# Kernel optimization log

Measured on AMD Instinct MI355X. Metric: run time of the kernel, lower is better.

The kernel has to match this reference:

```python
import jax, jax.numpy as jnp
import numpy as np

QK_DIM = 1024
V_DIM = 1024
NUM_HEADS = 16
HEAD_DIM = 64
INNER = NUM_HEADS * HEAD_DIM  # 1024
SCALE = HEAD_DIM ** -0.5


def setup_inputs() -> dict:
    key = jax.random.key(0)
    ks = jax.random.split(key, 8)
    m, nq, nkv = 4, 2048, 2048
    xq = jax.random.normal(ks[0], (m, nq, QK_DIM), dtype=jnp.float32)
    xk = jax.random.normal(ks[1], (m, nkv, QK_DIM), dtype=jnp.float32)
    xv = jax.random.normal(ks[2], (m, nkv, V_DIM), dtype=jnp.float32)
    # torch nn.Linear weights are [out, in]; y = x @ W.T
    s_qk = (QK_DIM) ** -0.5
    s_in = (INNER) ** -0.5
    Wq = jax.random.uniform(ks[3], (INNER, QK_DIM), jnp.float32, -s_qk, s_qk)
    Wk = jax.random.uniform(ks[4], (INNER, QK_DIM), jnp.float32, -s_qk, s_qk)
    Wv = jax.random.uniform(ks[5], (INNER, V_DIM), jnp.float32, -s_qk, s_qk)
    Wo = jax.random.uniform(ks[6], (V_DIM, INNER), jnp.float32, -s_in, s_in)
    bo = jax.random.uniform(ks[7], (V_DIM,), jnp.float32, -s_in, s_in)
    return {"xq": xq, "xk": xk, "xv": xv, "Wq": Wq, "Wk": Wk, "Wv": Wv, "Wo": Wo, "bo": bo}


def reference(xq, xk, xv, Wq, Wk, Wv, Wo, bo):
    m, nq, _ = xq.shape
    nkv = xk.shape[1]
    # projections (no bias), split heads: b n (h d) -> b h n d
    q = (xq @ Wq.T).reshape(m, nq, NUM_HEADS, HEAD_DIM).transpose(0, 2, 1, 3)
    k = (xk @ Wk.T).reshape(m, nkv, NUM_HEADS, HEAD_DIM).transpose(0, 2, 1, 3)
    v = (xv @ Wv.T).reshape(m, nkv, NUM_HEADS, HEAD_DIM).transpose(0, 2, 1, 3)
    dots = jnp.einsum("bhqd,bhkd->bhqk", q, k) * SCALE  # [m,h,nq,nkv]
    attn = jax.nn.softmax(dots, axis=-1)
    out = jnp.einsum("bhqk,bhkd->bhqd", attn, v)
    out = out.transpose(0, 2, 1, 3).reshape(m, nq, INNER)  # b h n d -> b n (h d)
    return out @ Wo.T + bo  # to_out Linear (dropout p=0 -> identity)
```

## Files before the change

### kernel.cpp

```cpp
#include <hip/hip_runtime.h>

typedef unsigned short u16;
using bf16x8 = __attribute__((ext_vector_type(8))) __bf16;
using f32x4  = __attribute__((ext_vector_type(4))) float;

#define QSCALE 0.18033688011f

#define EXP2F(x) __builtin_amdgcn_exp2f(x)

__device__ __forceinline__ u16 f2bf(float f) {
  union { float f; unsigned int u; } x; x.f = f;
  unsigned int r = x.u + 0x7FFFu + ((x.u >> 16) & 1u);
  return (u16)(r >> 16);
}

__device__ __forceinline__ bf16x8 ld8(const u16* p) {
  return *reinterpret_cast<const bf16x8*>(p);
}

__device__ __forceinline__ void gload16(const u16* g, u16* l) {
  __builtin_amdgcn_global_load_lds(
      (const __attribute__((address_space(1))) unsigned int*)g,
      (__attribute__((address_space(3))) unsigned int*)l, 16, 0, 0);
}

__global__ void cast3_f32_to_bf16(const float* __restrict__ a, const float* __restrict__ b,
                                  const float* __restrict__ c, u16* __restrict__ out, int n4) {
  const int y = blockIdx.y;
  const int i = blockIdx.x * 256 + threadIdx.x;
  if (i >= n4) return;
  const float* src = (y == 0) ? a : (y == 1) ? b : c;
  const float4 v = reinterpret_cast<const float4*>(src)[i];
  ushort4 o;
  o.x = f2bf(v.x); o.y = f2bf(v.y); o.z = f2bf(v.z); o.w = f2bf(v.w);
  reinterpret_cast<ushort4*>(out + (size_t)y * n4 * 4)[i] = o;
}

__global__ void cast4_f32_to_bf16(const float* __restrict__ a, const float* __restrict__ b,
                                  const float* __restrict__ c, const float* __restrict__ d,
                                  u16* __restrict__ out, int n4) {
  const int y = blockIdx.y;
  const int i = blockIdx.x * 256 + threadIdx.x;
  if (i >= n4) return;
  const float* src = (y == 0) ? a : (y == 1) ? b : (y == 2) ? c : d;
  const float4 v = reinterpret_cast<const float4*>(src)[i];
  ushort4 o;
  o.x = f2bf(v.x); o.y = f2bf(v.y); o.z = f2bf(v.z); o.w = f2bf(v.w);
  reinterpret_cast<ushort4*>(out + (size_t)y * n4 * 4)[i] = o;
}

#define GEMM_CORE(A_, B_, K_, BX_, BY_)                                              \
  __shared__ alignas(16) u16 lds_a[128 * 32];                                        \
  __shared__ alignas(16) u16 lds_b[128 * 32];                                        \
  const int t = threadIdx.x;                                                         \
  const int w = t >> 6, lane = t & 63;                                               \
  const int wr = w >> 1, wc = w & 1;                                                 \
  const size_t row0 = (size_t)(BY_) * 128;                                           \
  const size_t col0 = (size_t)(BX_) * 128;                                           \
  f32x4 acc[4][4];                                                                   \
  _Pragma("unroll") for (int i = 0; i < 4; ++i)                                      \
    _Pragma("unroll") for (int j = 0; j < 4; ++j) acc[i][j] = {0.f, 0.f, 0.f, 0.f};  \
  const u16* ga = A_ + (row0 + (t >> 2)) * K_ + (t & 3) * 8;                         \
  const u16* gb = B_ + (col0 + (t >> 2)) * K_ + (t & 3) * 8;                         \
  u16* la = lds_a + w * 512;                                                         \
  u16* lb = lds_b + w * 512;                                                         \
  const int fr = lane & 15;                                                          \
  const int fk = (lane >> 4) * 8;                                                    \
  for (int kt = 0; kt < K_; kt += 32) {                                              \
    __syncthreads();                                                                 \
    gload16(ga + kt, la);                                                            \
    gload16(ga + (size_t)64 * K_ + kt, la + 2048);                                   \
    gload16(gb + kt, lb);                                                            \
    gload16(gb + (size_t)64 * K_ + kt, lb + 2048);                                   \
    __syncthreads();                                                                 \
    bf16x8 af[4], bfr[4];                                                            \
    _Pragma("unroll") for (int i = 0; i < 4; ++i)                                    \
      af[i] = ld8(&lds_a[(wr * 64 + i * 16 + fr) * 32 + fk]);                        \
    _Pragma("unroll") for (int j = 0; j < 4; ++j)                                    \
      bfr[j] = ld8(&lds_b[(wc * 64 + j * 16 + fr) * 32 + fk]);                       \
    _Pragma("unroll") for (int i = 0; i < 4; ++i)                                    \
      _Pragma("unroll") for (int j = 0; j < 4; ++j)                                  \
        acc[i][j] = __builtin_amdgcn_mfma_f32_16x16x32_bf16(af[i], bfr[j], acc[i][j], 0, 0, 0); \
  }                                                                                  \
  const int er = (lane >> 4) * 4, ec = lane & 15;

__global__ __launch_bounds__(256)
void gemm_qkv(const u16* __restrict__ Aall, const u16* __restrict__ Ball,
              u16* __restrict__ Call) {
  const int g = (blockIdx.x & 7) * 192 + (blockIdx.x >> 3);
  const int bx = g & 7, by = (g >> 3) & 63, z = g >> 9;
  const u16* A = Aall + (size_t)z * 8192 * 1024;
  const u16* B = Ball + (size_t)z * 1024 * 1024;
  u16* C = Call + (size_t)z * 8192 * 1024;
  GEMM_CORE(A, B, 1024, bx, by)
#pragma unroll
  for (int i = 0; i < 4; ++i)
#pragma unroll
    for (int j = 0; j < 4; ++j) {
      const size_t row = row0 + wr * 64 + i * 16 + er;
      const size_t col = col0 + wc * 64 + j * 16 + ec;
      if (z == 0) {
#pragma unroll
        for (int r = 0; r < 4; ++r)
          C[(row + r) * 1024 + col] = f2bf(acc[i][j][r] * QSCALE);
      } else if (z == 1) {
#pragma unroll
        for (int r = 0; r < 4; ++r) {
          const size_t n = row + r;
          const size_t colswz = (col & ~(size_t)63) |
                                ((col & 63) ^ (((n & 7) << 3)));
          C[n * 1024 + colswz] = f2bf(acc[i][j][r]);
        }
      } else {
        ushort4 o4;
        o4.x = f2bf(acc[i][j][0]); o4.y = f2bf(acc[i][j][1]);
        o4.z = f2bf(acc[i][j][2]); o4.w = f2bf(acc[i][j][3]);
        const size_t nloc = row & 2047;
        const size_t d = col & 63;
        size_t pos = (nloc & ~(size_t)31) | (((nloc >> 2) & 3) << 3) |
                     (((nloc >> 4) & 1) << 2) | (nloc & 3);
        pos ^= (d & 7) << 3;
        const size_t idx = (((row >> 11) * 16 + (col >> 6)) * 64 + d) * 2048 + pos;
        *reinterpret_cast<ushort4*>(&C[idx]) = o4;
      }
    }
}

__global__ __launch_bounds__(256)
void gemm_out(const u16* __restrict__ A, const u16* __restrict__ B,
              float* __restrict__ Cf, const float* __restrict__ bias) {
  const int g = (blockIdx.x & 7) * 64 + (blockIdx.x >> 3);
  const int bx = g & 7, by = g >> 3;
  GEMM_CORE(A, B, 1024, bx, by)
#pragma unroll
  for (int i = 0; i < 4; ++i)
#pragma unroll
    for (int j = 0; j < 4; ++j) {
      const size_t row = row0 + wr * 64 + i * 16 + er;
      const size_t col = col0 + wc * 64 + j * 16 + ec;
#pragma unroll
      for (int r = 0; r < 4; ++r)
        Cf[(row + r) * 1024 + col] = acc[i][j][r] + bias[col];
    }
}

__global__ __launch_bounds__(512)
void flash_attn(const u16* __restrict__ Q, const u16* __restrict__ Km,
                const u16* __restrict__ Vt, u16* __restrict__ O) {
  const int o_blk = (blockIdx.x & 7) * 64 + (blockIdx.x >> 3);
  const int qt = o_blk & 7, h = (o_blk >> 3) & 15, b = o_blk >> 7;
  const int t = threadIdx.x;
  const int w = t >> 6, lane = t & 63;
  const int l16 = lane & 15, lh = lane >> 4;

  __shared__ alignas(16) u16 kt_lds[2][64][64];
  __shared__ alignas(16) u16 vt_lds[2][64][64];

  const size_t base_qk = ((size_t)b * 2048) * 1024 + (size_t)h * 64;
  const size_t base_vt = ((size_t)(b * 16 + h)) * 64 * 2048;

  bf16x8 qf[2][2];
#pragma unroll
  for (int g = 0; g < 2; ++g) {
    const size_t qrow = (size_t)qt * 256 + (w * 2 + g) * 16 + l16;
    const u16* qp = Q + base_qk + qrow * 1024 + lh * 8;
    qf[g][0] = ld8(qp);
    qf[g][1] = ld8(qp + 32);
  }

  bf16x8 vones;
#pragma unroll
  for (int i = 0; i < 8; ++i) vones[i] = (__bf16)1.0f;

  f32x4 o_acc[2][4];
  f32x4 o_sum[2];
#pragma unroll
  for (int g = 0; g < 2; ++g) {
#pragma unroll
    for (int j = 0; j < 4; ++j) o_acc[g][j] = {0.f, 0.f, 0.f, 0.f};
    o_sum[g] = {0.f, 0.f, 0.f, 0.f};
  }

  const int srow = t >> 3;
  const int schk = (t & 7) * 8;
  const u16* kg = Km + base_qk + (size_t)srow * 1024 + schk;
  const u16* vg = Vt + base_vt + (size_t)srow * 2048 + schk;
  u16* kl0 = &kt_lds[0][0][0] + w * 512;
  u16* kl1 = &kt_lds[1][0][0] + w * 512;
  u16* vl0 = &vt_lds[0][0][0] + w * 512;
  u16* vl1 = &vt_lds[1][0][0] + w * 512;

  gload16(kg, kl0);
  gload16(vg, vl0);

  const int xo = (l16 & 7) << 3;

  for (int it = 0; it < 32; ++it) {
    const int cur = it & 1;
    __syncthreads();

    if (it != 31) {
      const int nkv = (it + 1) * 64;
      gload16(kg + (size_t)nkv * 1024, cur ? kl0 : kl1);
      gload16(vg + nkv, cur ? vl0 : vl1);
    }

    f32x4 s[2][4];
#pragma unroll
    for (int g = 0; g < 2; ++g)
#pragma unroll
      for (int j = 0; j < 4; ++j) s[g][j] = {0.f, 0.f, 0.f, 0.f};
    __builtin_amdgcn_s_setprio(1);
#pragma unroll
    for (int j = 0; j < 4; ++j)
#pragma unroll
      for (int ks = 0; ks < 2; ++ks) {
        bf16x8 kf = ld8(&kt_lds[cur][j * 16 + l16][(ks * 32 + lh * 8) ^ xo]);
        s[0][j] = __builtin_amdgcn_mfma_f32_16x16x32_bf16(kf, qf[0][ks], s[0][j], 0, 0, 0);
        s[1][j] = __builtin_amdgcn_mfma_f32_16x16x32_bf16(kf, qf[1][ks], s[1][j], 0, 0, 0);
      }
    __builtin_amdgcn_s_setprio(0);

    bf16x8 pa[2][2];
#pragma unroll
    for (int g = 0; g < 2; ++g)
#pragma unroll
      for (int j = 0; j < 4; ++j)
#pragma unroll
        for (int r = 0; r < 4; ++r)
          s[g][j][r] = EXP2F(s[g][j][r]);
#pragma unroll
    for (int g = 0; g < 2; ++g)
#pragma unroll
      for (int c = 0; c < 2; ++c)
#pragma unroll
        for (int i = 0; i < 8; ++i)
          pa[g][c][i] = (__bf16)s[g][2 * c + (i >> 2)][i & 3];

    __builtin_amdgcn_s_setprio(1);
#pragma unroll
    for (int c = 0; c < 2; ++c) {
      o_sum[0] = __builtin_amdgcn_mfma_f32_16x16x32_bf16(pa[0][c], vones, o_sum[0], 0, 0, 0);
      o_sum[1] = __builtin_amdgcn_mfma_f32_16x16x32_bf16(pa[1][c], vones, o_sum[1], 0, 0, 0);
#pragma unroll
      for (int jd = 0; jd < 4; ++jd) {
        bf16x8 vf = ld8(&vt_lds[cur][jd * 16 + l16][(c * 32 + lh * 8) ^ xo]);
        o_acc[0][jd] = __builtin_amdgcn_mfma_f32_16x16x32_bf16(pa[0][c], vf, o_acc[0][jd], 0, 0, 0);
        o_acc[1][jd] = __builtin_amdgcn_mfma_f32_16x16x32_bf16(pa[1][c], vf, o_acc[1][jd], 0, 0, 0);
      }
    }
    __builtin_amdgcn_s_setprio(0);
  }

#pragma unroll
  for (int g = 0; g < 2; ++g) {
    float linv[4];
#pragma unroll
    for (int r = 0; r < 4; ++r) linv[r] = 1.0f / o_sum[g][r];
    const size_t orow0 = (size_t)b * 2048 + (size_t)qt * 256 + (w * 2 + g) * 16;
#pragma unroll
    for (int jd = 0; jd < 4; ++jd) {
      const int col = h * 64 + jd * 16 + l16;
#pragma unroll
      for (int r = 0; r < 4; ++r)
        O[(orow0 + lh * 4 + r) * 1024 + col] = f2bf(o_acc[g][jd][r] * linv[r]);
    }
  }
}

extern "C" void kernel_launch(void* const* d_in, const int* in_sizes, int n_in,
                              void* d_out, int out_size, void* d_ws, size_t ws_size,
                              hipStream_t stream) {
  const float* xq = (const float*)d_in[0];
  const float* xk = (const float*)d_in[1];
  const float* xv = (const float*)d_in[2];
  const float* Wq = (const float*)d_in[3];
  const float* Wk = (const float*)d_in[4];
  const float* Wv = (const float*)d_in[5];
  const float* Wo = (const float*)d_in[6];
  const float* bo = (const float*)d_in[7];
  float* out = (float*)d_out;

  const size_t X = (size_t)8192 * 1024;
  const size_t W = (size_t)1024 * 1024;

  u16* p = (u16*)d_ws;
  u16* x_bf  = p; p += 3 * X;
  u16* w_bf  = p; p += 4 * W;
  u16* qkv   = p; p += 3 * X;
  u16* attn_bf = x_bf;

  dim3 blk(256);
  cast3_f32_to_bf16<<<dim3(8192, 3), blk, 0, stream>>>(xq, xk, xv, x_bf, (int)(X / 4));
  cast4_f32_to_bf16<<<dim3(1024, 4), blk, 0, stream>>>(Wq, Wk, Wv, Wo, w_bf, (int)(W / 4));

  gemm_qkv<<<dim3(1536), blk, 0, stream>>>(x_bf, w_bf, qkv);

  flash_attn<<<dim3(512), dim3(512), 0, stream>>>(qkv, qkv + X, qkv + 2 * X, attn_bf);

  gemm_out<<<dim3(512), blk, 0, stream>>>(attn_bf, w_bf + 3 * W, out, bo);
}
```

Measured before the change: 193.9 us.

## Deepen GEMM K-tile to 64 with XOR-swizzled LDS and fence flash-attn loads

Both projection GEMMs now stage a 128x64 K-slice per iteration instead of 128x32. That halves the number of barrier round-trips and gives each wave two MFMA sub-steps per sync. LDS rows are written and read with an XOR-swizzled 8-element chunk index to avoid bank conflicts, and the LDS footprint per block doubles. The attention loop adds an explicit vmcnt(0) wait and scheduler barriers around the sync and prefetch, so async LDS loads are guaranteed complete and the compiler cannot reorder across them.

```diff
diff --git a/kernel.cpp b/kernel.cpp
--- a/kernel.cpp
+++ b/kernel.cpp
@@ -7,6 +7,7 @@
 #define QSCALE 0.18033688011f
 
 #define EXP2F(x) __builtin_amdgcn_exp2f(x)
+#define SCHED_FENCE() __builtin_amdgcn_sched_barrier(0)
 
 __device__ __forceinline__ u16 f2bf(float f) {
   union { float f; unsigned int u; } x; x.f = f;
@@ -18,7 +19,7 @@
   return *reinterpret_cast<const bf16x8*>(p);
 }
 
-__device__ __forceinline__ void gload16(const u16* g, u16* l) {
+__device__ __forceinline__ void gload16(const void* g, void* l) {
   __builtin_amdgcn_global_load_lds(
       (const __attribute__((address_space(1))) unsigned int*)g,
       (__attribute__((address_space(3))) unsigned int*)l, 16, 0, 0);
@@ -49,38 +50,41 @@
   reinterpret_cast<ushort4*>(out + (size_t)y * n4 * 4)[i] = o;
 }
 
-#define GEMM_CORE(A_, B_, K_, BX_, BY_)                                              \
-  __shared__ alignas(16) u16 lds_a[128 * 32];                                        \
-  __shared__ alignas(16) u16 lds_b[128 * 32];                                        \
+#define GEMM64_BODY(A_, B_)                                                          \
+  __shared__ alignas(16) u16 lds_a[128 * 64];                                        \
+  __shared__ alignas(16) u16 lds_b[128 * 64];                                        \
   const int t = threadIdx.x;                                                         \
   const int w = t >> 6, lane = t & 63;                                               \
   const int wr = w >> 1, wc = w & 1;                                                 \
-  const size_t row0 = (size_t)(BY_) * 128;                                           \
-  const size_t col0 = (size_t)(BX_) * 128;                                           \
   f32x4 acc[4][4];                                                                   \
   _Pragma("unroll") for (int i = 0; i < 4; ++i)                                      \
     _Pragma("unroll") for (int j = 0; j < 4; ++j) acc[i][j] = {0.f, 0.f, 0.f, 0.f};  \
-  const u16* ga = A_ + (row0 + (t >> 2)) * K_ + (t & 3) * 8;                         \
-  const u16* gb = B_ + (col0 + (t >> 2)) * K_ + (t & 3) * 8;                         \
-  u16* la = lds_a + w * 512;                                                         \
-  u16* lb = lds_b + w * 512;                                                         \
+  const int b_r = t >> 3;                                                            \
+  const int b_c = ((t & 7) ^ (b_r & 7)) * 8;                                         \
+  const u16* gaa = A_ + (row0 + b_r) * 1024 + b_c;                                   \
+  const u16* gbb = B_ + (col0 + b_r) * 1024 + b_c;                                   \
   const int fr = lane & 15;                                                          \
-  const int fk = (lane >> 4) * 8;                                                    \
-  for (int kt = 0; kt < K_; kt += 32) {                                              \
+  const int flh = lane >> 4;                                                         \
+  const int fx7 = fr & 7;                                                            \
+  for (int kt = 0; kt < 1024; kt += 64) {                                            \
     __syncthreads();                                                                 \
-    gload16(ga + kt, la);                                                            \
-    gload16(ga + (size_t)64 * K_ + kt, la + 2048);                                   \
-    gload16(gb + kt, lb);                                                            \
-    gload16(gb + (size_t)64 * K_ + kt, lb + 2048);                                   \
+    _Pragma("unroll") for (int s = 0; s < 4; ++s) {                                  \
+      gload16(gaa + (size_t)(32 * s) * 1024 + kt, lds_a + s * 2048 + w * 512);       \
+      gload16(gbb + (size_t)(32 * s) * 1024 + kt, lds_b + s * 2048 + w * 512);       \
+    }                                                                                \
+    asm volatile("s_waitcnt vmcnt(0)" ::: "memory");                                 \
     __syncthreads();                                                                 \
-    bf16x8 af[4], bfr[4];                                                            \
-    _Pragma("unroll") for (int i = 0; i < 4; ++i)                                    \
-      af[i] = ld8(&lds_a[(wr * 64 + i * 16 + fr) * 32 + fk]);                        \
-    _Pragma("unroll") for (int j = 0; j < 4; ++j)                                    \
-      bfr[j] = ld8(&lds_b[(wc * 64 + j * 16 + fr) * 32 + fk]);                       \
-    _Pragma("unroll") for (int i = 0; i < 4; ++i)                                    \
+    _Pragma("unroll") for (int ks2 = 0; ks2 < 2; ++ks2) {                            \
+      bf16x8 af[4], bfr[4];                                                          \
+      const int gch = ks2 * 4 + flh;                                                 \
+      _Pragma("unroll") for (int i = 0; i < 4; ++i)                                  \
+        af[i] = ld8(&lds_a[(wr * 64 + i * 16 + fr) * 64 + ((gch ^ fx7) * 8)]);       \
       _Pragma("unroll") for (int j = 0; j < 4; ++j)                                  \
-        acc[i][j] = __builtin_amdgcn_mfma_f32_16x16x32_bf16(af[i], bfr[j], acc[i][j], 0, 0, 0); \
+        bfr[j] = ld8(&lds_b[(wc * 64 + j * 16 + fr) * 64 + ((gch ^ fx7) * 8)]);      \
+      _Pragma("unroll") for (int i = 0; i < 4; ++i)                                  \
+        _Pragma("unroll") for (int j = 0; j < 4; ++j)                                \
+          acc[i][j] = __builtin_amdgcn_mfma_f32_16x16x32_bf16(af[i], bfr[j], acc[i][j], 0, 0, 0); \
+    }                                                                                \
   }                                                                                  \
   const int er = (lane >> 4) * 4, ec = lane & 15;
 
@@ -92,7 +96,11 @@
   const u16* A = Aall + (size_t)z * 8192 * 1024;
   const u16* B = Ball + (size_t)z * 1024 * 1024;
   u16* C = Call + (size_t)z * 8192 * 1024;
-  GEMM_CORE(A, B, 1024, bx, by)
+  const size_t row0 = (size_t)by * 128;
+  const size_t col0 = (size_t)bx * 128;
+
+  GEMM64_BODY(A, B)
+
 #pragma unroll
   for (int i = 0; i < 4; ++i)
 #pragma unroll
@@ -131,7 +139,11 @@
               float* __restrict__ Cf, const float* __restrict__ bias) {
   const int g = (blockIdx.x & 7) * 64 + (blockIdx.x >> 3);
   const int bx = g & 7, by = g >> 3;
-  GEMM_CORE(A, B, 1024, bx, by)
+  const size_t row0 = (size_t)by * 128;
+  const size_t col0 = (size_t)bx * 128;
+
+  GEMM64_BODY(A, B)
+
 #pragma unroll
   for (int i = 0; i < 4; ++i)
 #pragma unroll
@@ -197,13 +209,17 @@
 
   for (int it = 0; it < 32; ++it) {
     const int cur = it & 1;
+    asm volatile("s_waitcnt vmcnt(0)" ::: "memory");
+    SCHED_FENCE();
     __syncthreads();
+    SCHED_FENCE();
 
     if (it != 31) {
       const int nkv = (it + 1) * 64;
       gload16(kg + (size_t)nkv * 1024, cur ? kl0 : kl1);
       gload16(vg + nkv, cur ? vl0 : vl1);
     }
+    SCHED_FENCE();
 
     f32x4 s[2][4];
 #pragma unroll
```

Result: faster. 184.0 us (-5.1%).
